# Kernel tuning notes

Hardware: AMD Instinct MI355X
Metric: run time of the kernel (lower is better)

## Reference

```python
import jax, jax.numpy as jnp
import numpy as np

D = 768          # embed_dim
NH = 12          # num_heads
HD = D // NH     # head_dim = 64
DEPTH = 12
PATCH = 16
IMG = 256
NP_ = (IMG // PATCH) ** 2   # 256 spatial patches
PTOT = NP_ + 1              # 257 tokens per frame (cls + patches)
SCALE = HD ** -0.5
EPS = 1e-5


def _attn(xb, w, b):
    # xb: (B, S, D); w: (D, 3D); b: (3D,)
    B, S, _ = xb.shape
    qkv = (xb @ w + b).reshape(B, S, 3, NH, HD).transpose(2, 0, 3, 1, 4)
    q, k, v = qkv[0], qkv[1], qkv[2]             # each (B, NH, S, HD)
    a = jax.nn.softmax(jnp.einsum('bhqd,bhkd->bhqk', q, k) * SCALE, axis=-1)
    o = jnp.einsum('bhqk,bhkd->bhqd', a, v)      # (B, NH, S, HD)
    return o.transpose(0, 2, 1, 3).reshape(B, S, D)


def setup_inputs() -> dict:
    key = jax.random.key(0)
    ks = jax.random.split(key, 16)
    std = 0.02
    inp = {
        'x': jax.random.normal(ks[0], (2, 16, 3, IMG, IMG), jnp.float32),
        'patch_w': jax.random.normal(ks[1], (D, 3, PATCH, PATCH), jnp.float32) * std,
        'patch_b': jnp.zeros((D,), jnp.float32),
        'cls_token': jax.random.normal(ks[2], (1, 1, D), jnp.float32) * std,
        'pos_embed': jax.random.normal(ks[3], (1, PTOT, D), jnp.float32) * std,
        'time_embed': jax.random.normal(ks[4], (1, 16, D), jnp.float32) * std,
        'wqkv_s': jax.random.normal(ks[5], (DEPTH, D, 3 * D), jnp.float32) * std,
        'bqkv_s': jnp.zeros((DEPTH, 3 * D), jnp.float32),
        'wqkv_t': jax.random.normal(ks[6], (DEPTH, D, 3 * D), jnp.float32) * std,
        'bqkv_t': jnp.zeros((DEPTH, 3 * D), jnp.float32),
        'wproj': jax.random.normal(ks[7], (DEPTH, D, D), jnp.float32) * std,
        'bproj': jnp.zeros((DEPTH, D), jnp.float32),
        'ln_g': jnp.ones((D,), jnp.float32),
        'ln_b': jnp.zeros((D,), jnp.float32),
        'head_w': jax.random.normal(ks[8], (1, D), jnp.float32) * std,
        'head_b': jnp.zeros((1,), jnp.float32),
    }
    return inp


def reference(x, patch_w, patch_b, cls_token, pos_embed, time_embed,
              wqkv_s, bqkv_s, wqkv_t, bqkv_t, wproj, bproj,
              ln_g, ln_b, head_w, head_b):
    N, T, C, H, W = x.shape
    Hp = H // PATCH
    # patch embed: 16x16 stride-16 conv as unfold + matmul
    xp = x.reshape(N * T, C, Hp, PATCH, Hp, PATCH)
    xp = xp.transpose(0, 2, 4, 1, 3, 5).reshape(N * T, NP_, C * PATCH * PATCH)
    tok = xp @ patch_w.reshape(D, -1).T + patch_b          # (N*T, 256, D)
    tok = tok.reshape(N, T, NP_, D)
    cls = jnp.broadcast_to(cls_token, (N, T, 1, D))
    h = jnp.concatenate([cls, tok], axis=2)                # (N, T, 257, D)
    h = h + pos_embed[:, None]                             # (1,1,257,D) broadcast
    h = h + time_embed[:, :T][:, :, None]                  # (1,T,1,D) broadcast
    h = h.reshape(N, T * PTOT, D)

    for i in range(DEPTH):
        x4 = h.reshape(N, T, PTOT, D)
        # spatial attention within each frame
        xs = x4.reshape(N * T, PTOT, D)
        so = _attn(xs, wqkv_s[i], bqkv_s[i]) @ wproj[i] + bproj[i]
        x4 = x4 + so.reshape(N, T, PTOT, D)
        # temporal attention across frames per spatial location
        xt = x4.transpose(0, 2, 1, 3).reshape(N * PTOT, T, D)
        to = _attn(xt, wqkv_t[i], bqkv_t[i]) @ wproj[i] + bproj[i]
        x4 = x4 + to.reshape(N, PTOT, T, D).transpose(0, 2, 1, 3)
        h = x4.reshape(N, T * PTOT, D)

    mu = h.mean(axis=-1, keepdims=True)
    var = ((h - mu) ** 2).mean(axis=-1, keepdims=True)
    h = (h - mu) * jax.lax.rsqrt(var + EPS) * ln_g + ln_b
    cls_tok = h.reshape(N, T, PTOT, D)[:, :, 0, :].mean(axis=1)   # (N, D)
    logits = cls_tok @ head_w.T + head_b                          # (N, 1)
    return logits
```

## Files before the change

kernel.cpp:

```cpp
#include <hip/hip_runtime.h>
#include <hip/hip_bf16.h>
#include <math.h>

namespace {

constexpr int D    = 768;
constexpr int NH   = 12;
constexpr int PTOT = 257;
constexpr int NB   = 2;
constexpr int TT   = 16;
constexpr int NTOK = NB * TT * PTOT;
constexpr int NPAT = NB * TT * 256;
constexpr int QKVD = 3 * D;

typedef short short8  __attribute__((ext_vector_type(8)));
typedef float float4v __attribute__((ext_vector_type(4)));

__device__ __forceinline__ float bf2f(unsigned short u) {
  unsigned v = ((unsigned)u) << 16;
  float f; __builtin_memcpy(&f, &v, 4); return f;
}
__device__ __forceinline__ unsigned short f2bf(float f) {
  unsigned u; __builtin_memcpy(&u, &f, 4);
  u += 0x7FFFu + ((u >> 16) & 1u);
  return (unsigned short)(u >> 16);
}

__device__ __forceinline__ void gload_lds16(const void* g, void* l) {
  __builtin_amdgcn_global_load_lds((const __attribute__((address_space(1))) void*)g,
                                   (__attribute__((address_space(3))) void*)l, 16, 0, 0);
}

__global__ __launch_bounds__(256) void unfold_kernel(const float* __restrict__ x,
                                                     unsigned short* __restrict__ xpb) {
  int idx = blockIdx.x * 256 + threadIdx.x;
  if (idx >= NPAT * D) return;
  int f  = idx % D;
  int pg = idx / D;
  int c = f >> 8;
  int r = f & 255;
  int i = r >> 4, j = r & 15;
  int nt = pg >> 8;
  int s  = pg & 255;
  int hp = s >> 4, wp = s & 15;
  xpb[idx] = f2bf(x[(size_t)(nt * 3 + c) * 65536 + (size_t)(hp * 16 + i) * 256 + (wp * 16 + j)]);
}

__global__ __launch_bounds__(256) void cast_pw(const float* __restrict__ pw,
                                               unsigned short* __restrict__ pwb) {
  int idx = blockIdx.x * 256 + threadIdx.x;
  if (idx >= D * D) return;
  pwb[idx] = f2bf(pw[idx]);
}

__global__ __launch_bounds__(256) void wconv(const float* __restrict__ W,
                                             unsigned short* __restrict__ WT, int N) {
  __shared__ float tile[32][33];
  int l = blockIdx.z;
  const float* w = W + (size_t)l * 768 * N;
  unsigned short* wt = WT + (size_t)l * 768 * N;
  int n0 = blockIdx.x * 32, k0 = blockIdx.y * 32;
  int t = threadIdx.x;
  {
    int r = t >> 3, c4 = (t & 7) * 4;
    float4 v = *(const float4*)(w + (size_t)(k0 + r) * N + n0 + c4);
    tile[r][c4 + 0] = v.x; tile[r][c4 + 1] = v.y;
    tile[r][c4 + 2] = v.z; tile[r][c4 + 3] = v.w;
  }
  __syncthreads();
  {
    int rn = t >> 3, ck = (t & 7) * 4;
    ushort4 o;
    o.x = f2bf(tile[ck + 0][rn]); o.y = f2bf(tile[ck + 1][rn]);
    o.z = f2bf(tile[ck + 2][rn]); o.w = f2bf(tile[ck + 3][rn]);
    *(ushort4*)(wt + (size_t)(n0 + rn) * 768 + k0 + ck) = o;
  }
}

__global__ __launch_bounds__(256) void assemble_kernel(const float* __restrict__ tok,
    const float* __restrict__ cls,
    const float* __restrict__ pos, const float* __restrict__ tim,
    float* __restrict__ h, unsigned short* __restrict__ hb) {
  int idx = blockIdx.x * 256 + threadIdx.x;
  if (idx >= NTOK * D) return;
  int d = idx % D;
  int tokid = idx / D;
  int p  = tokid % PTOT;
  int nt = tokid / PTOT;
  int t  = nt % TT;
  float v = pos[p * D + d] + tim[t * D + d];
  if (p == 0) v += cls[d];
  else        v += tok[(size_t)(nt * 256 + (p - 1)) * D + d];
  h[idx] = v;
  hb[idx] = f2bf(v);
}

__global__ __launch_bounds__(256) void gemm_bf16(
    const unsigned short* __restrict__ A,
    const unsigned short* __restrict__ BT,
    const float* __restrict__ bias,
    unsigned short* __restrict__ Cb,
    float* __restrict__ Hf,
    unsigned short* __restrict__ Hb,
    int M, int N, int mode)
{
  constexpr int K = 768;
  constexpr int NT = K / 32;
  __shared__ unsigned short smem[16384];
  auto As = (unsigned short (*)[128][32])smem;
  auto Bs = (unsigned short (*)[128][32])(smem + 8192);
  auto Ct = (unsigned short (*)[128])smem;
  int tid = threadIdx.x;

  int nwg = gridDim.x * gridDim.y;
  int wg  = blockIdx.y * gridDim.x + blockIdx.x;
  int qq  = nwg >> 3, rr = nwg & 7;
  int xcd = wg & 7, bidx = wg >> 3;
  int newid = (xcd < rr ? xcd * (qq + 1) : rr * (qq + 1) + (xcd - rr) * qq) + bidx;
  int m0 = (newid / gridDim.x) * 128;
  int n0 = (newid % gridDim.x) * 128;

  int w = tid >> 6, lane = tid & 63;
  int quad = lane >> 4, l16 = lane & 15;
  int wm = (w & 1) * 64, wn = (w >> 1) * 64;
  const int lrow = lane >> 2;
  const int scol = (lane & 3) * 8;
  float4v acc[4][4] = {};

  const unsigned short* gA0 = A + (size_t)min(m0 + w * 32 + lrow, M - 1) * K + scol;
  const unsigned short* gA1 = A + (size_t)min(m0 + w * 32 + 16 + lrow, M - 1) * K + scol;
  const unsigned short* gB0 = BT + (size_t)(n0 + w * 32 + lrow) * K + scol;
  const unsigned short* gB1 = BT + (size_t)(n0 + w * 32 + 16 + lrow) * K + scol;

  auto STAGE = [&](int buf, int t) {
    int kk = t * 32;
    gload_lds16(gA0 + kk, &As[buf][w * 32][0]);
    gload_lds16(gA1 + kk, &As[buf][w * 32 + 16][0]);
    gload_lds16(gB0 + kk, &Bs[buf][w * 32][0]);
    gload_lds16(gB1 + kk, &Bs[buf][w * 32 + 16][0]);
  };
  auto COMPUTE = [&](int buf) {
    short8 af[4], bfr[4];
    #pragma unroll
    for (int i = 0; i < 4; ++i) {
      af[i]  = *(const short8*)&As[buf][wm + i * 16 + l16][quad * 8];
      bfr[i] = *(const short8*)&Bs[buf][wn + i * 16 + l16][quad * 8];
    }
    __builtin_amdgcn_s_setprio(1);
    #pragma unroll
    for (int i = 0; i < 4; ++i)
      #pragma unroll
      for (int j = 0; j < 4; ++j)
        acc[i][j] = __builtin_amdgcn_mfma_f32_16x16x32_bf16(af[i], bfr[j], acc[i][j], 0, 0, 0);
    __builtin_amdgcn_s_setprio(0);
  };

  STAGE(0, 0);
  __syncthreads();
  for (int t = 0; t < NT; t += 2) {
    STAGE(1, t + 1);
    COMPUTE(0);
    __syncthreads();
    if (t + 2 < NT) STAGE(0, t + 2);
    COMPUTE(1);
    __syncthreads();
  }

  if (mode == 2) {
    #pragma unroll
    for (int j = 0; j < 4; ++j) {
      int col = n0 + wn + j * 16 + l16;
      float bv = bias[col];
      #pragma unroll
      for (int i = 0; i < 4; ++i) {
        #pragma unroll
        for (int r = 0; r < 4; ++r) {
          int row = m0 + wm + i * 16 + quad * 4 + r;
          if (row < M) Hf[(size_t)row * N + col] = acc[i][j][r] + bv;
        }
      }
    }
    return;
  }

  #pragma unroll
  for (int j = 0; j < 4; ++j) {
    int col = wn + j * 16 + l16;
    float bv = bias[n0 + col];
    int pc = (((col >> 3) ^ quad) << 3) | (col & 7);
    #pragma unroll
    for (int i = 0; i < 4; ++i) {
      #pragma unroll
      for (int r = 0; r < 4; ++r) {
        int row = wm + i * 16 + quad * 4 + r;
        float v = acc[i][j][r] + bv;
        unsigned short ov;
        if (mode == 1) {
          size_t off = (size_t)(m0 + row) * N + (n0 + col);
          if (m0 + row < M) {
            float nv = Hf[off] + v;
            Hf[off] = nv;
            ov = f2bf(nv);
          } else ov = 0;
        } else {
          ov = f2bf(v);
        }
        Ct[row][pc] = ov;
      }
    }
  }
  __syncthreads();
  unsigned short* Ob = (mode == 0) ? Cb : Hb;
  #pragma unroll
  for (int e = 0; e < 8; ++e) {
    int c    = e * 256 + tid;
    int trow = c >> 4, tch = c & 15;
    int grow = m0 + trow;
    if (grow < M) {
      int pch = tch ^ ((trow >> 2) & 3);
      *(uint4*)(Ob + (size_t)grow * N + n0 + tch * 8) = *(const uint4*)&Ct[trow][pch * 8];
    }
  }
}

__global__ __launch_bounds__(256) void gemm_bf16_h64(
    const unsigned short* __restrict__ A,
    const unsigned short* __restrict__ BT,
    const float* __restrict__ bias,
    unsigned short* __restrict__ Cb,
    int M, int N)
{
  constexpr int K = 768;
  constexpr int NT = K / 32;
  __shared__ unsigned short smem[12288];
  auto As = (unsigned short (*)[64][32])smem;
  auto Bs = (unsigned short (*)[128][32])(smem + 4096);
  auto Ct = (unsigned short (*)[128])smem;
  int tid = threadIdx.x;

  int nwg = gridDim.x * gridDim.y;
  int wg  = blockIdx.y * gridDim.x + blockIdx.x;
  int qq  = nwg >> 3, rr = nwg & 7;
  int xcd = wg & 7, bidx = wg >> 3;
  int newid = (xcd < rr ? xcd * (qq + 1) : rr * (qq + 1) + (xcd - rr) * qq) + bidx;
  int m0 = (newid / gridDim.x) * 64;
  int n0 = (newid % gridDim.x) * 128;

  int w = tid >> 6, lane = tid & 63;
  int quad = lane >> 4, l16 = lane & 15;
  int wm = (w & 1) * 32, wn = (w >> 1) * 64;
  const int lrow = lane >> 2;
  const int scol = (lane & 3) * 8;
  float4v acc[2][4] = {};

  const unsigned short* gA0 = A + (size_t)min(m0 + w * 16 + lrow, M - 1) * K + scol;
  const unsigned short* gB0 = BT + (size_t)(n0 + w * 32 + lrow) * K + scol;
  const unsigned short* gB1 = BT + (size_t)(n0 + w * 32 + 16 + lrow) * K + scol;

  auto STAGE = [&](int buf, int t) {
    int kk = t * 32;
    gload_lds16(gA0 + kk, &As[buf][w * 16][0]);
    gload_lds16(gB0 + kk, &Bs[buf][w * 32][0]);
    gload_lds16(gB1 + kk, &Bs[buf][w * 32 + 16][0]);
  };
  auto COMPUTE = [&](int buf) {
    short8 af[2], bfr[4];
    #pragma unroll
    for (int i = 0; i < 2; ++i)
      af[i] = *(const short8*)&As[buf][wm + i * 16 + l16][quad * 8];
    #pragma unroll
    for (int j = 0; j < 4; ++j)
      bfr[j] = *(const short8*)&Bs[buf][wn + j * 16 + l16][quad * 8];
    __builtin_amdgcn_s_setprio(1);
    #pragma unroll
    for (int i = 0; i < 2; ++i)
      #pragma unroll
      for (int j = 0; j < 4; ++j)
        acc[i][j] = __builtin_amdgcn_mfma_f32_16x16x32_bf16(af[i], bfr[j], acc[i][j], 0, 0, 0);
    __builtin_amdgcn_s_setprio(0);
  };

  STAGE(0, 0);
  __syncthreads();
  for (int t = 0; t < NT; t += 2) {
    STAGE(1, t + 1);
    COMPUTE(0);
    __syncthreads();
    if (t + 2 < NT) STAGE(0, t + 2);
    COMPUTE(1);
    __syncthreads();
  }

  #pragma unroll
  for (int j = 0; j < 4; ++j) {
    int col = wn + j * 16 + l16;
    float bv = bias[n0 + col];
    int pc = (((col >> 3) ^ quad) << 3) | (col & 7);
    #pragma unroll
    for (int i = 0; i < 2; ++i) {
      #pragma unroll
      for (int r = 0; r < 4; ++r) {
        int row = wm + i * 16 + quad * 4 + r;
        Ct[row][pc] = f2bf(acc[i][j][r] + bv);
      }
    }
  }
  __syncthreads();
  #pragma unroll
  for (int e = 0; e < 4; ++e) {
    int c = e * 256 + tid;
    int trow = c >> 4, tch = c & 15;
    int grow = m0 + trow;
    if (grow < M) {
      int pch = tch ^ ((trow >> 2) & 3);
      *(uint4*)(Cb + (size_t)grow * N + n0 + tch * 8) = *(const uint4*)&Ct[trow][pch * 8];
    }
  }
}

__global__ __launch_bounds__(256) void attn_spatial3(
    const unsigned short* __restrict__ qkv,
    unsigned short* __restrict__ o)
{
  __shared__ unsigned short Qs[64][72];
  __shared__ unsigned short KVs[64][72];
  __shared__ unsigned short Psl[4][16][72];
  int tid = threadIdx.x;
  int w = tid >> 6, lane = tid & 63;
  int quad = lane >> 4, l16 = lane & 15;
  int bid = blockIdx.x;
  int bh = bid / 5, qt = bid % 5;
  int nt = bh / NH, head = bh % NH;
  int q0 = qt * 64;
  size_t base = (size_t)nt * PTOT;
  const unsigned short* Qg = qkv + head * 64;
  const unsigned short* Kg = qkv + 768 + head * 64;
  const unsigned short* Vg = qkv + 1536 + head * 64;

  #pragma unroll
  for (int e = 0; e < 2; ++e) {
    int chunk = e * 256 + tid;
    int row = chunk >> 3, off = (chunk & 7) * 8;
    int qr = min(q0 + row, PTOT - 1);
    *(uint4*)&Qs[row][off] = *(const uint4*)(Qg + (base + qr) * (size_t)QKVD + off);
  }
  __syncthreads();
  int qrow = w * 16 + l16;
  short8 qa0 = *(const short8*)&Qs[qrow][quad * 8];
  short8 qa1 = *(const short8*)&Qs[qrow][32 + quad * 8];

  float4v st[17];
  #pragma unroll
  for (int kc = 0; kc < 5; ++kc) {
    __syncthreads();
    #pragma unroll
    for (int e = 0; e < 2; ++e) {
      int chunk = e * 256 + tid;
      int row = chunk >> 3, off = (chunk & 7) * 8;
      int kr = min(kc * 64 + row, PTOT - 1);
      *(uint4*)&KVs[row][off] = *(const uint4*)(Kg + (base + kr) * (size_t)QKVD + off);
    }
    __syncthreads();
    #pragma unroll
    for (int tt = 0; tt < 4; ++tt) {
      int t = kc * 4 + tt;
      if (t < 17) {
        short8 kb0 = *(const short8*)&KVs[tt * 16 + l16][quad * 8];
        short8 kb1 = *(const short8*)&KVs[tt * 16 + l16][32 + quad * 8];
        float4v a = {0.f, 0.f, 0.f, 0.f};
        a = __builtin_amdgcn_mfma_f32_16x16x32_bf16(qa0, kb0, a, 0, 0, 0);
        a = __builtin_amdgcn_mfma_f32_16x16x32_bf16(qa1, kb1, a, 0, 0, 0);
        st[t] = a;
      }
    }
  }
  if (l16 >= 1) {
    st[16][0] = -1e30f; st[16][1] = -1e30f; st[16][2] = -1e30f; st[16][3] = -1e30f;
  }
  float mx[4] = {-1e30f, -1e30f, -1e30f, -1e30f};
  #pragma unroll
  for (int t = 0; t < 17; ++t)
    #pragma unroll
    for (int r = 0; r < 4; ++r) mx[r] = fmaxf(mx[r], st[t][r]);
  #pragma unroll
  for (int off = 1; off < 16; off <<= 1)
    #pragma unroll
    for (int r = 0; r < 4; ++r) mx[r] = fmaxf(mx[r], __shfl_xor(mx[r], off));
  float sm[4] = {0.f, 0.f, 0.f, 0.f};
  #pragma unroll
  for (int t = 0; t < 17; ++t)
    #pragma unroll
    for (int r = 0; r < 4; ++r) {
      float e = __expf((st[t][r] - mx[r]) * 0.125f);
      st[t][r] = e;
      sm[r] += e;
    }
  #pragma unroll
  for (int off = 1; off < 16; off <<= 1)
    #pragma unroll
    for (int r = 0; r < 4; ++r) sm[r] += __shfl_xor(sm[r], off);
  float linv[4];
  #pragma unroll
  for (int r = 0; r < 4; ++r) linv[r] = 1.f / sm[r];

  float4v oacc[4] = {};
  #pragma unroll
  for (int vc = 0; vc < 5; ++vc) {
    __syncthreads();
    #pragma unroll
    for (int e = 0; e < 2; ++e) {
      int chunk = e * 256 + tid;
      int row = chunk >> 3;
      int oo  = chunk & 7;
      int off = oo * 8;
      int vr = min(vc * 64 + row, PTOT - 1);
      uint4 u = *(const uint4*)(Vg + (base + vr) * (size_t)QKVD + off);
      #pragma unroll
      for (int s = 0; s < 8; ++s) {
        int idx = (oo + s) & 7;
        unsigned sel01 = (idx & 2) ? u.y : u.x;
        unsigned sel23 = (idx & 2) ? u.w : u.z;
        unsigned dw    = (idx & 4) ? sel23 : sel01;
        unsigned short val = (idx & 1) ? (unsigned short)(dw >> 16) : (unsigned short)dw;
        KVs[off + idx][row] = val;
      }
    }
    #pragma unroll
    for (int tt = 0; tt < 4; ++tt) {
      int t = vc * 4 + tt;
      #pragma unroll
      for (int r = 0; r < 4; ++r) {
        unsigned short pv = 0;
        if (t < 17) pv = f2bf(st[t][r]);
        Psl[w][quad * 4 + r][tt * 16 + l16] = pv;
      }
    }
    __syncthreads();
    int ksmax = (vc == 4) ? 1 : 2;
    #pragma unroll
    for (int ks = 0; ks < 2; ++ks) {
      if (ks < ksmax) {
        short8 pa = *(const short8*)&Psl[w][l16][ks * 32 + quad * 8];
        #pragma unroll
        for (int j = 0; j < 4; ++j) {
          short8 vb = *(const short8*)&KVs[j * 16 + l16][ks * 32 + quad * 8];
          oacc[j] = __builtin_amdgcn_mfma_f32_16x16x32_bf16(pa, vb, oacc[j], 0, 0, 0);
        }
      }
    }
  }
  #pragma unroll
  for (int r = 0; r < 4; ++r) {
    int qg = q0 + w * 16 + quad * 4 + r;
    if (qg < PTOT) {
      #pragma unroll
      for (int j = 0; j < 4; ++j)
        o[(base + qg) * (size_t)D + head * 64 + j * 16 + l16] = f2bf(oacc[j][r] * linv[r]);
    }
  }
}

__global__ __launch_bounds__(256) void attn_temporal2(const unsigned short* __restrict__ qkv,
                                                      unsigned short* __restrict__ o) {
  __shared__ unsigned short Ps[4][16][32];
  __shared__ unsigned short VT[4][64][32];
  int tid = threadIdx.x;
  int w = tid >> 6, lane = tid & 63;
  int quad = lane >> 4, l16 = lane & 15;
  int s = blockIdx.x * 4 + w;
  int p  = s % PTOT;
  int nh = s / PTOT;
  int n = nh / NH, head = nh % NH;

  {
    ushort4 z = {0, 0, 0, 0};
    *(ushort4*)&Ps[w][lane >> 2][16 + (lane & 3) * 4] = z;
    *(uint4*)&VT[w][lane][16] = (uint4){0, 0, 0, 0};
    *(uint4*)&VT[w][lane][24] = (uint4){0, 0, 0, 0};
  }

  const size_t rstride = (size_t)PTOT * QKVD;
  const unsigned short* base0 = qkv + ((size_t)(n * TT) * PTOT + p) * QKVD + head * 64;

  const unsigned short* qrow = base0 + (size_t)l16 * rstride;
  short8 qa0 = *(const short8*)(qrow + quad * 8);
  short8 qa1 = *(const short8*)(qrow + 32 + quad * 8);
  const unsigned short* krow = qrow + 768;
  short8 kb0 = *(const short8*)(krow + quad * 8);
  short8 kb1 = *(const short8*)(krow + 32 + quad * 8);

  float4v sc = {0.f, 0.f, 0.f, 0.f};
  sc = __builtin_amdgcn_mfma_f32_16x16x32_bf16(qa0, kb0, sc, 0, 0, 0);
  sc = __builtin_amdgcn_mfma_f32_16x16x32_bf16(qa1, kb1, sc, 0, 0, 0);

  float e4[4], mx[4], sm[4];
  #pragma unroll
  for (int r = 0; r < 4; ++r) mx[r] = sc[r] * 0.125f;
  #pragma unroll
  for (int off = 1; off < 16; off <<= 1)
    #pragma unroll
    for (int r = 0; r < 4; ++r) mx[r] = fmaxf(mx[r], __shfl_xor(mx[r], off));
  #pragma unroll
  for (int r = 0; r < 4; ++r) { e4[r] = __expf(sc[r] * 0.125f - mx[r]); sm[r] = e4[r]; }
  #pragma unroll
  for (int off = 1; off < 16; off <<= 1)
    #pragma unroll
    for (int r = 0; r < 4; ++r) sm[r] += __shfl_xor(sm[r], off);
  float linv[4];
  #pragma unroll
  for (int r = 0; r < 4; ++r) linv[r] = 1.f / sm[r];

  #pragma unroll
  for (int r = 0; r < 4; ++r) Ps[w][quad * 4 + r][l16] = f2bf(e4[r]);

  {
    const unsigned short* vrow = qrow + 1536 + quad * 16;
    uint4 v0 = *(const uint4*)vrow;
    uint4 v1 = *(const uint4*)(vrow + 8);
    const unsigned short* pv0 = (const unsigned short*)&v0;
    const unsigned short* pv1 = (const unsigned short*)&v1;
    #pragma unroll
    for (int i = 0; i < 8; ++i) VT[w][quad * 16 + i][l16]     = pv0[i];
    #pragma unroll
    for (int i = 0; i < 8; ++i) VT[w][quad * 16 + 8 + i][l16] = pv1[i];
  }

  short8 pa = *(const short8*)&Ps[w][l16][quad * 8];
  float4v oacc[4];
  #pragma unroll
  for (int j = 0; j < 4; ++j) {
    short8 vb = *(const short8*)&VT[w][j * 16 + l16][quad * 8];
    float4v z = {0.f, 0.f, 0.f, 0.f};
    oacc[j] = __builtin_amdgcn_mfma_f32_16x16x32_bf16(pa, vb, z, 0, 0, 0);
  }

  #pragma unroll
  for (int r = 0; r < 4; ++r) {
    size_t orow = ((size_t)(n * TT + quad * 4 + r) * PTOT + p) * D + head * 64;
    #pragma unroll
    for (int j = 0; j < 4; ++j)
      o[orow + j * 16 + l16] = f2bf(oacc[j][r] * linv[r]);
  }
}

__device__ __forceinline__ float block_sum(float v, float* lds) {
  #pragma unroll
  for (int off = 32; off; off >>= 1) v += __shfl_down(v, off);
  __syncthreads();
  if ((threadIdx.x & 63) == 0) lds[threadIdx.x >> 6] = v;
  __syncthreads();
  return lds[0] + lds[1] + lds[2] + lds[3];
}

__global__ __launch_bounds__(256) void head_kernel(const float* __restrict__ h,
    const float* __restrict__ g, const float* __restrict__ b,
    const float* __restrict__ hw, const float* __restrict__ hb,
    float* __restrict__ out) {
  __shared__ float lds[4];
  int n = blockIdx.x, tid = threadIdx.x;
  float logit = 0.f;
  for (int t = 0; t < TT; ++t) {
    const float* row = h + (size_t)((n * TT + t) * PTOT) * D;
    float v[3]; float s = 0.f;
    #pragma unroll
    for (int i = 0; i < 3; ++i) { v[i] = row[tid + 256 * i]; s += v[i]; }
    s = block_sum(s, lds);
    float mu = s * (1.f / D);
    float s2 = 0.f;
    #pragma unroll
    for (int i = 0; i < 3; ++i) { float d0 = v[i] - mu; s2 += d0 * d0; }
    s2 = block_sum(s2, lds);
    float rstd = rsqrtf(s2 * (1.f / D) + 1e-5f);
    float dot = 0.f;
    #pragma unroll
    for (int i = 0; i < 3; ++i) {
      int d0 = tid + 256 * i;
      float y = (v[i] - mu) * rstd * g[d0] + b[d0];
      dot += y * hw[d0];
    }
    dot = block_sum(dot, lds);
    logit += dot;
  }
  if (tid == 0) out[n] = logit * (1.f / TT) + hb[0];
}

}

extern "C" void kernel_launch(void* const* d_in, const int* in_sizes, int n_in,
                              void* d_out, int out_size, void* d_ws, size_t ws_size,
                              hipStream_t stream) {
  const float* x       = (const float*)d_in[0];
  const float* patch_w = (const float*)d_in[1];
  const float* patch_b = (const float*)d_in[2];
  const float* cls     = (const float*)d_in[3];
  const float* pos     = (const float*)d_in[4];
  const float* tim     = (const float*)d_in[5];
  const float* wqkv_s  = (const float*)d_in[6];
  const float* bqkv_s  = (const float*)d_in[7];
  const float* wqkv_t  = (const float*)d_in[8];
  const float* bqkv_t  = (const float*)d_in[9];
  const float* wproj   = (const float*)d_in[10];
  const float* bproj   = (const float*)d_in[11];
  const float* ln_g    = (const float*)d_in[12];
  const float* ln_b    = (const float*)d_in[13];
  const float* head_w  = (const float*)d_in[14];
  const float* head_b  = (const float*)d_in[15];
  float* out = (float*)d_out;

  char* p = (char*)d_ws;
  float* h = (float*)p;                 p += (size_t)NTOK * D * 4;
  unsigned short* hb = (unsigned short*)p;   p += (size_t)NTOK * D * 2;
  unsigned short* qkvb = (unsigned short*)p; p += (size_t)NTOK * QKVD * 2;
  unsigned short* ob = (unsigned short*)p;   p += (size_t)NTOK * D * 2;
  unsigned short* wsT = (unsigned short*)p;  p += (size_t)12 * QKVD * D * 2;
  unsigned short* wtT = (unsigned short*)p;  p += (size_t)12 * QKVD * D * 2;
  unsigned short* wpT = (unsigned short*)p;  p += (size_t)12 * D * D * 2;
  unsigned short* xpb = qkvb;
  unsigned short* pwb = ob;
  float* tok = (float*)wsT;

  unfold_kernel<<<(NPAT * D + 255) / 256, 256, 0, stream>>>(x, xpb);
  cast_pw<<<(D * D + 255) / 256, 256, 0, stream>>>(patch_w, pwb);
  gemm_bf16<<<dim3(D / 128, NPAT / 128), 256, 0, stream>>>(
      xpb, pwb, patch_b, nullptr, tok, nullptr, NPAT, D, 2);
  assemble_kernel<<<(NTOK * D + 255) / 256, 256, 0, stream>>>(tok, cls, pos, tim, h, hb);

  wconv<<<dim3(QKVD / 32, D / 32, 12), 256, 0, stream>>>(wqkv_s, wsT, QKVD);
  wconv<<<dim3(QKVD / 32, D / 32, 12), 256, 0, stream>>>(wqkv_t, wtT, QKVD);
  wconv<<<dim3(D / 32, D / 32, 12), 256, 0, stream>>>(wproj, wpT, D);

  const int MB = (NTOK + 127) / 128;
  const int MB64 = (NTOK + 63) / 64;
  for (int l = 0; l < 12; ++l) {
    gemm_bf16_h64<<<dim3(QKVD / 128, MB64), 256, 0, stream>>>(
        hb, wsT + (size_t)l * QKVD * D, bqkv_s + (size_t)l * QKVD,
        qkvb, NTOK, QKVD);
    attn_spatial3<<<NB * TT * NH * 5, 256, 0, stream>>>(qkvb, ob);
    gemm_bf16<<<dim3(D / 128, MB), 256, 0, stream>>>(
        ob, wpT + (size_t)l * D * D, bproj + (size_t)l * D,
        nullptr, h, hb, NTOK, D, 1);

    gemm_bf16_h64<<<dim3(QKVD / 128, MB64), 256, 0, stream>>>(
        hb, wtT + (size_t)l * QKVD * D, bqkv_t + (size_t)l * QKVD,
        qkvb, NTOK, QKVD);
    attn_temporal2<<<(NB * NH * PTOT) / 4, 256, 0, stream>>>(qkvb, ob);
    gemm_bf16<<<dim3(D / 128, MB), 256, 0, stream>>>(
        ob, wpT + (size_t)l * D * D, bproj + (size_t)l * D,
        nullptr, h, hb, NTOK, D, 1);
  }

  head_kernel<<<2, 256, 0, stream>>>(h, ln_g, ln_b, head_w, head_b, out);
}
```

Measured before the change: 3.081 ms.

## Use 128x128 QKV GEMM tiles with triple-buffered LDS pipeline and split head

The QKV projection GEMM goes from a 64x128 tile with double buffering and two full barriers per iteration to a 128x128 tile with three LDS buffers. Loads are issued two steps ahead, with manual vmcnt waits and a single barrier per k-step. The larger tile halves the workgroup count and reuses each B tile across more rows, at the cost of more LDS and accumulator registers per block. The final head is also split into a 32-block per-frame LayerNorm/dot kernel plus a tiny reduction kernel, replacing the serial 2-block loop.

```diff
diff --git a/kernel.cpp b/kernel.cpp
--- a/kernel.cpp
+++ b/kernel.cpp
@@ -223,7 +223,7 @@
   }
 }
 
-__global__ __launch_bounds__(256) void gemm_bf16_h64(
+__global__ __launch_bounds__(256) void gemm_bf16_p3(
     const unsigned short* __restrict__ A,
     const unsigned short* __restrict__ BT,
     const float* __restrict__ bias,
@@ -232,9 +232,9 @@
 {
   constexpr int K = 768;
   constexpr int NT = K / 32;
-  __shared__ unsigned short smem[12288];
-  auto As = (unsigned short (*)[64][32])smem;
-  auto Bs = (unsigned short (*)[128][32])(smem + 4096);
+  __shared__ unsigned short smem[24576];
+  auto As = (unsigned short (*)[128][32])smem;
+  auto Bs = (unsigned short (*)[128][32])(smem + 12288);
   auto Ct = (unsigned short (*)[128])smem;
   int tid = threadIdx.x;
 
@@ -243,53 +243,62 @@
   int qq  = nwg >> 3, rr = nwg & 7;
   int xcd = wg & 7, bidx = wg >> 3;
   int newid = (xcd < rr ? xcd * (qq + 1) : rr * (qq + 1) + (xcd - rr) * qq) + bidx;
-  int m0 = (newid / gridDim.x) * 64;
+  int m0 = (newid / gridDim.x) * 128;
   int n0 = (newid % gridDim.x) * 128;
 
   int w = tid >> 6, lane = tid & 63;
   int quad = lane >> 4, l16 = lane & 15;
-  int wm = (w & 1) * 32, wn = (w >> 1) * 64;
+  int wm = (w & 1) * 64, wn = (w >> 1) * 64;
   const int lrow = lane >> 2;
   const int scol = (lane & 3) * 8;
-  float4v acc[2][4] = {};
-
-  const unsigned short* gA0 = A + (size_t)min(m0 + w * 16 + lrow, M - 1) * K + scol;
+  float4v acc[4][4] = {};
+
+  const unsigned short* gA0 = A + (size_t)min(m0 + w * 32 + lrow, M - 1) * K + scol;
+  const unsigned short* gA1 = A + (size_t)min(m0 + w * 32 + 16 + lrow, M - 1) * K + scol;
   const unsigned short* gB0 = BT + (size_t)(n0 + w * 32 + lrow) * K + scol;
   const unsigned short* gB1 = BT + (size_t)(n0 + w * 32 + 16 + lrow) * K + scol;
 
   auto STAGE = [&](int buf, int t) {
     int kk = t * 32;
-    gload_lds16(gA0 + kk, &As[buf][w * 16][0]);
+    gload_lds16(gA0 + kk, &As[buf][w * 32][0]);
+    gload_lds16(gA1 + kk, &As[buf][w * 32 + 16][0]);
     gload_lds16(gB0 + kk, &Bs[buf][w * 32][0]);
     gload_lds16(gB1 + kk, &Bs[buf][w * 32 + 16][0]);
   };
   auto COMPUTE = [&](int buf) {
-    short8 af[2], bfr[4];
-    #pragma unroll
-    for (int i = 0; i < 2; ++i)
-      af[i] = *(const short8*)&As[buf][wm + i * 16 + l16][quad * 8];
-    #pragma unroll
-    for (int j = 0; j < 4; ++j)
-      bfr[j] = *(const short8*)&Bs[buf][wn + j * 16 + l16][quad * 8];
+    short8 af[4], bfr[4];
+    #pragma unroll
+    for (int i = 0; i < 4; ++i) {
+      af[i]  = *(const short8*)&As[buf][wm + i * 16 + l16][quad * 8];
+      bfr[i] = *(const short8*)&Bs[buf][wn + i * 16 + l16][quad * 8];
+    }
     __builtin_amdgcn_s_setprio(1);
     #pragma unroll
-    for (int i = 0; i < 2; ++i)
+    for (int i = 0; i < 4; ++i)
       #pragma unroll
       for (int j = 0; j < 4; ++j)
         acc[i][j] = __builtin_amdgcn_mfma_f32_16x16x32_bf16(af[i], bfr[j], acc[i][j], 0, 0, 0);
     __builtin_amdgcn_s_setprio(0);
   };
+  auto STEP = [&](int t, int buf, int bufp2) {
+    if (t < NT - 1) { asm volatile("s_waitcnt vmcnt(4)" ::: "memory"); }
+    else            { asm volatile("s_waitcnt vmcnt(0)" ::: "memory"); }
+    __builtin_amdgcn_s_barrier();
+    asm volatile("" ::: "memory");
+    if (t + 2 < NT) STAGE(bufp2, t + 2);
+    COMPUTE(buf);
+  };
 
   STAGE(0, 0);
-  __syncthreads();
-  for (int t = 0; t < NT; t += 2) {
-    STAGE(1, t + 1);
-    COMPUTE(0);
-    __syncthreads();
-    if (t + 2 < NT) STAGE(0, t + 2);
-    COMPUTE(1);
-    __syncthreads();
-  }
+  STAGE(1, 1);
+  #pragma unroll 1
+  for (int t0 = 0; t0 < NT; t0 += 3) {
+    STEP(t0 + 0, 0, 2);
+    STEP(t0 + 1, 1, 0);
+    STEP(t0 + 2, 2, 1);
+  }
+  __builtin_amdgcn_sched_barrier(0);
+  __syncthreads();
 
   #pragma unroll
   for (int j = 0; j < 4; ++j) {
@@ -297,7 +306,7 @@
     float bv = bias[n0 + col];
     int pc = (((col >> 3) ^ quad) << 3) | (col & 7);
     #pragma unroll
-    for (int i = 0; i < 2; ++i) {
+    for (int i = 0; i < 4; ++i) {
       #pragma unroll
       for (int r = 0; r < 4; ++r) {
         int row = wm + i * 16 + quad * 4 + r;
@@ -307,8 +316,8 @@
   }
   __syncthreads();
   #pragma unroll
-  for (int e = 0; e < 4; ++e) {
-    int c = e * 256 + tid;
+  for (int e = 0; e < 8; ++e) {
+    int c    = e * 256 + tid;
     int trow = c >> 4, tch = c & 15;
     int grow = m0 + trow;
     if (grow < M) {
@@ -552,36 +561,41 @@
   return lds[0] + lds[1] + lds[2] + lds[3];
 }
 
-__global__ __launch_bounds__(256) void head_kernel(const float* __restrict__ h,
+__global__ __launch_bounds__(256) void head1_kernel(const float* __restrict__ h,
     const float* __restrict__ g, const float* __restrict__ b,
-    const float* __restrict__ hw, const float* __restrict__ hb,
-    float* __restrict__ out) {
+    const float* __restrict__ hw, float* __restrict__ scratch) {
   __shared__ float lds[4];
-  int n = blockIdx.x, tid = threadIdx.x;
-  float logit = 0.f;
-  for (int t = 0; t < TT; ++t) {
-    const float* row = h + (size_t)((n * TT + t) * PTOT) * D;
-    float v[3]; float s = 0.f;
-    #pragma unroll
-    for (int i = 0; i < 3; ++i) { v[i] = row[tid + 256 * i]; s += v[i]; }
-    s = block_sum(s, lds);
-    float mu = s * (1.f / D);
-    float s2 = 0.f;
-    #pragma unroll
-    for (int i = 0; i < 3; ++i) { float d0 = v[i] - mu; s2 += d0 * d0; }
-    s2 = block_sum(s2, lds);
-    float rstd = rsqrtf(s2 * (1.f / D) + 1e-5f);
-    float dot = 0.f;
-    #pragma unroll
-    for (int i = 0; i < 3; ++i) {
-      int d0 = tid + 256 * i;
-      float y = (v[i] - mu) * rstd * g[d0] + b[d0];
-      dot += y * hw[d0];
-    }
-    dot = block_sum(dot, lds);
-    logit += dot;
-  }
-  if (tid == 0) out[n] = logit * (1.f / TT) + hb[0];
+  int nt = blockIdx.x, tid = threadIdx.x;
+  const float* row = h + (size_t)(nt * PTOT) * D;
+  float v[3]; float s = 0.f;
+  #pragma unroll
+  for (int i = 0; i < 3; ++i) { v[i] = row[tid + 256 * i]; s += v[i]; }
+  s = block_sum(s, lds);
+  float mu = s * (1.f / D);
+  float s2 = 0.f;
+  #pragma unroll
+  for (int i = 0; i < 3; ++i) { float d0 = v[i] - mu; s2 += d0 * d0; }
+  s2 = block_sum(s2, lds);
+  float rstd = rsqrtf(s2 * (1.f / D) + 1e-5f);
+  float dot = 0.f;
+  #pragma unroll
+  for (int i = 0; i < 3; ++i) {
+    int d0 = tid + 256 * i;
+    float y = (v[i] - mu) * rstd * g[d0] + b[d0];
+    dot += y * hw[d0];
+  }
+  dot = block_sum(dot, lds);
+  if (tid == 0) scratch[nt] = dot;
+}
+
+__global__ __launch_bounds__(64) void head2_kernel(const float* __restrict__ scratch,
+    const float* __restrict__ hb_, float* __restrict__ out) {
+  int lane = threadIdx.x;
+  float v = (lane < NB * TT) ? scratch[lane] : 0.f;
+  #pragma unroll
+  for (int off = 1; off < 16; off <<= 1) v += __shfl_xor(v, off);
+  if (lane == 0)  out[0] = v * (1.f / TT) + hb_[0];
+  if (lane == 16) out[1] = v * (1.f / TT) + hb_[0];
 }
 
 }
@@ -618,6 +632,7 @@
   unsigned short* xpb = qkvb;
   unsigned short* pwb = ob;
   float* tok = (float*)wsT;
+  float* scratch = (float*)ob;
 
   unfold_kernel<<<(NPAT * D + 255) / 256, 256, 0, stream>>>(x, xpb);
   cast_pw<<<(D * D + 255) / 256, 256, 0, stream>>>(patch_w, pwb);
@@ -630,9 +645,8 @@
   wconv<<<dim3(D / 32, D / 32, 12), 256, 0, stream>>>(wproj, wpT, D);
 
   const int MB = (NTOK + 127) / 128;
-  const int MB64 = (NTOK + 63) / 64;
   for (int l = 0; l < 12; ++l) {
-    gemm_bf16_h64<<<dim3(QKVD / 128, MB64), 256, 0, stream>>>(
+    gemm_bf16_p3<<<dim3(QKVD / 128, MB), 256, 0, stream>>>(
         hb, wsT + (size_t)l * QKVD * D, bqkv_s + (size_t)l * QKVD,
         qkvb, NTOK, QKVD);
     attn_spatial3<<<NB * TT * NH * 5, 256, 0, stream>>>(qkvb, ob);
@@ -640,7 +654,7 @@
         ob, wpT + (size_t)l * D * D, bproj + (size_t)l * D,
         nullptr, h, hb, NTOK, D, 1);
 
-    gemm_bf16_h64<<<dim3(QKVD / 128, MB64), 256, 0, stream>>>(
+    gemm_bf16_p3<<<dim3(QKVD / 128, MB), 256, 0, stream>>>(
         hb, wtT + (size_t)l * QKVD * D, bqkv_t + (size_t)l * QKVD,
         qkvb, NTOK, QKVD);
     attn_temporal2<<<(NB * NH * PTOT) / 4, 256, 0, stream>>>(qkvb, ob);
@@ -649,5 +663,6 @@
         nullptr, h, hb, NTOK, D, 1);
   }
 
-  head_kernel<<<2, 256, 0, stream>>>(h, ln_g, ln_b, head_w, head_b, out);
-}
+  head1_kernel<<<NB * TT, 256, 0, stream>>>(h, ln_g, ln_b, head_w, scratch);
+  head2_kernel<<<1, 64, 0, stream>>>(scratch, head_b, out);
+}
```

Result: faster. 2.767 ms (median of 2 runs) (-10.2%).
